# Performance work log

Measured on AMD Instinct MI355X. Metric: run time of the kernel, lower is better.

Reference implementation:

```python
import jax, jax.numpy as jnp
import numpy as np

N = 80
MAX_ITERS = 60   # fixed unroll; per-pair convergence handled by masking
TOL = 1e-3       # matches torch |ev - ev_new| < 0.001


def setup_inputs() -> dict:
    key = jax.random.key(0)
    k1, k2, k3, k4, k5, k6 = jax.random.split(key, 6)
    return {
        "x": jax.random.normal(k1, (N, 1), dtype=jnp.float32),
        "r_zeros": jax.random.uniform(k2, (N, N, N, N), dtype=jnp.float32),
        "r_const": jax.random.uniform(k3, (N, N, N, N), dtype=jnp.float32),
        "t_paths": jax.random.uniform(k4, (N, N), dtype=jnp.float32),
        "weights_t": jax.random.uniform(k5, (N, N), dtype=jnp.float32),
        "weights_r": jax.random.uniform(k6, (N, N, N, N), dtype=jnp.float32),
    }


def _batched_power_iteration(A):
    # A: [P, n, n]. Power iteration per pair, freezing converged pairs.
    P, n, _ = A.shape
    v0 = jnp.full((P, n), 1.0 / np.sqrt(n), dtype=A.dtype)

    def ev_fn(v):
        Av = jnp.einsum('pij,pj->pi', A, v)
        return jnp.einsum('pi,pi->p', v, Av)

    ev0 = ev_fn(v0)
    done0 = jnp.zeros((P,), dtype=bool)

    def body(carry, _):
        v, ev, done = carry
        Av = jnp.einsum('pij,pj->pi', A, v)
        v_new = Av / jnp.linalg.norm(Av, axis=1, keepdims=True)
        ev_new = ev_fn(v_new)
        conv = jnp.abs(ev - ev_new) < TOL
        # torch returns v_new at the converging step, then breaks
        v = jnp.where(done[:, None], v, v_new)
        ev = jnp.where(done, ev, ev_new)
        done = done | conv
        return (v, ev, done), None

    (v, ev, done), _ = jax.lax.scan(body, (v0, ev0, done0), None, length=MAX_ITERS)
    return ev, v


def reference(x, r_zeros, r_const, t_paths, weights_t, weights_r):
    n = x.shape[0]
    weights_t_fixed = weights_t * t_paths                      # [n, n]
    weights_r_comb = weights_r * r_zeros + r_const             # [n, n, n, n]

    A = weights_r_comb.reshape(n * n, n, n)                    # one matrix per (s,t)
    T_val = weights_t_fixed.reshape(n * n)                     # scalar per (s,t)
    src = jnp.repeat(jnp.arange(n), n)                         # s index per pair

    _, v = _batched_power_iteration(A)                         # [P, n]
    # compute_eigenvector_values: v / v[src] * T_val
    v_src = v[jnp.arange(n * n), src]                          # [P]
    deltas = v * (T_val / v_src)[:, None]                      # [P, n]
    rbc_arr = jnp.sum(deltas, axis=0)                          # [n]
    return rbc_arr
```

## Files before the change

### kernel.cpp

```cpp
#include <hip/hip_runtime.h>

#define NN 80
#define NPAIR (NN * NN)
#define MAXIT 60
#define TOLV 1e-3f

__device__ __forceinline__ float block_reduce_sum(float part, float* red) {
    const int lane = threadIdx.x & 63;
    const int wid  = threadIdx.x >> 6;
#pragma unroll
    for (int off = 32; off > 0; off >>= 1)
        part += __shfl_down(part, off, 64);
    if (lane == 0) red[wid] = part;
    __syncthreads();
    float r = red[0] + red[1] + red[2] + red[3];
    __syncthreads();
    return r;
}

template <bool ATOMIC>
__global__ __launch_bounds__(256) void pair_kernel(
    const float* __restrict__ r_zeros,
    const float* __restrict__ r_const,
    const float* __restrict__ t_paths,
    const float* __restrict__ weights_t,
    const float* __restrict__ weights_r,
    float* __restrict__ outbuf)
{
    __shared__ float A[NN][NN + 1];
    __shared__ float v[NN];
    __shared__ float Av[NN];
    __shared__ float red[4];

    const int p   = blockIdx.x;
    const int tid = threadIdx.x;
    const long base = (long)p * (NN * NN);

    const float4* wr4 = (const float4*)(weights_r + base);
    const float4* rz4 = (const float4*)(r_zeros + base);
    const float4* rc4 = (const float4*)(r_const + base);
    for (int c = tid; c < (NN * NN) / 4; c += 256) {
        float4 a = wr4[c];
        float4 b = rz4[c];
        float4 d = rc4[c];
        const int f = c * 4;
        const int row = f / NN, col = f % NN;
        A[row][col + 0] = fmaf(a.x, b.x, d.x);
        A[row][col + 1] = fmaf(a.y, b.y, d.y);
        A[row][col + 2] = fmaf(a.z, b.z, d.z);
        A[row][col + 3] = fmaf(a.w, b.w, d.w);
    }
    if (tid < NN) v[tid] = 0.11180339887498949f;
    __syncthreads();

    if (tid < NN) {
        float s = 0.f;
#pragma unroll
        for (int j = 0; j < NN; ++j) s = fmaf(A[tid][j], v[j], s);
        Av[tid] = s;
    }
    __syncthreads();
    float part = (tid < NN) ? v[tid] * Av[tid] : 0.f;
    float ev = block_reduce_sum(part, red);

    for (int it = 0; it < MAXIT; ++it) {
        part = (tid < NN) ? Av[tid] * Av[tid] : 0.f;
        const float inv = 1.f / sqrtf(block_reduce_sum(part, red));
        if (tid < NN) v[tid] = Av[tid] * inv;
        __syncthreads();
        if (tid < NN) {
            float s = 0.f;
#pragma unroll
            for (int j = 0; j < NN; ++j) s = fmaf(A[tid][j], v[j], s);
            Av[tid] = s;
        }
        __syncthreads();
        part = (tid < NN) ? v[tid] * Av[tid] : 0.f;
        const float ev_new = block_reduce_sum(part, red);
        if (fabsf(ev - ev_new) < TOLV) break;
        ev = ev_new;
    }

    const int s_idx = p / NN;
    const float T = weights_t[p] * t_paths[p];
    const float scale = T / v[s_idx];
    if (tid < NN) {
        const float dv = v[tid] * scale;
        if (ATOMIC) atomicAdd(&outbuf[tid], dv);
        else        outbuf[(long)p * NN + tid] = dv;
    }
}

__global__ __launch_bounds__(256) void reduce_kernel(
    const float* __restrict__ deltas, float* __restrict__ out)
{
    __shared__ float red[4];
    const int j = blockIdx.x;
    float part = 0.f;
    for (int p = threadIdx.x; p < NPAIR; p += 256)
        part += deltas[(long)p * NN + j];
    const int lane = threadIdx.x & 63;
    const int wid  = threadIdx.x >> 6;
#pragma unroll
    for (int off = 32; off > 0; off >>= 1)
        part += __shfl_down(part, off, 64);
    if (lane == 0) red[wid] = part;
    __syncthreads();
    if (threadIdx.x == 0) out[j] = red[0] + red[1] + red[2] + red[3];
}

extern "C" void kernel_launch(void* const* d_in, const int* in_sizes, int n_in,
                              void* d_out, int out_size, void* d_ws, size_t ws_size,
                              hipStream_t stream) {
    const float* r_zeros   = (const float*)d_in[1];
    const float* r_const   = (const float*)d_in[2];
    const float* t_paths   = (const float*)d_in[3];
    const float* weights_t = (const float*)d_in[4];
    const float* weights_r = (const float*)d_in[5];
    float* out = (float*)d_out;

    const size_t need = (size_t)NPAIR * NN * sizeof(float);
    if (ws_size >= need) {
        float* deltas = (float*)d_ws;
        pair_kernel<false><<<NPAIR, 256, 0, stream>>>(
            r_zeros, r_const, t_paths, weights_t, weights_r, deltas);
        reduce_kernel<<<NN, 256, 0, stream>>>(deltas, out);
    } else {
        hipMemsetAsync(d_out, 0, NN * sizeof(float), stream);
        pair_kernel<true><<<NPAIR, 256, 0, stream>>>(
            r_zeros, r_const, t_paths, weights_t, weights_r, out);
    }
}
```

Before: 443.5 us.

## Persistent double-buffered pair kernel overlapping next-matrix loads with power iteration

Replaces one-block-per-pair launch with a persistent grid of 768 blocks that loop over pairs, double-buffering the next pair's combined matrix in shared memory and interleaving chunks of its global load into the power-iteration steps. The matvec uses float4 reads with a rotated start index to avoid bank conflicts, and the two reductions per iteration are merged into one pass that also yields the norm for the next step. Results are accumulated with atomics instead of a workspace plus reduce kernel. The goal is to hide the HBM load latency behind the latency-bound iteration, at the cost of double shared memory and reduced occupancy.

```diff
diff --git a/kernel.cpp b/kernel.cpp
--- a/kernel.cpp
+++ b/kernel.cpp
@@ -1,112 +1,143 @@
 #include <hip/hip_runtime.h>
 
 #define NN 80
-#define NPAIR (NN * NN)
+#define NP4 1600
+#define NPAIR 6400
 #define MAXIT 60
 #define TOLV 1e-3f
+#define GRID 768
+#define NCHUNK 7
 
-__device__ __forceinline__ float block_reduce_sum(float part, float* red) {
-    const int lane = threadIdx.x & 63;
-    const int wid  = threadIdx.x >> 6;
+__device__ __forceinline__ float matvec_row(const float4* __restrict__ Ar4,
+                                            const float4* __restrict__ v4,
+                                            int q0) {
+    float s0 = 0.f, s1 = 0.f, s2 = 0.f, s3 = 0.f;
+    int q = q0;
 #pragma unroll
-    for (int off = 32; off > 0; off >>= 1)
-        part += __shfl_down(part, off, 64);
-    if (lane == 0) red[wid] = part;
-    __syncthreads();
-    float r = red[0] + red[1] + red[2] + red[3];
-    __syncthreads();
-    return r;
+    for (int c = 0; c < 20; ++c) {
+        const float4 a = Ar4[q];
+        const float4 w = v4[q];
+        s0 = fmaf(a.x, w.x, s0);
+        s1 = fmaf(a.y, w.y, s1);
+        s2 = fmaf(a.z, w.z, s2);
+        s3 = fmaf(a.w, w.w, s3);
+        q = (q == 19) ? 0 : q + 1;
+    }
+    return (s0 + s1) + (s2 + s3);
 }
 
-template <bool ATOMIC>
-__global__ __launch_bounds__(256) void pair_kernel(
+__global__ __launch_bounds__(256, 3) void pair_kernel(
     const float* __restrict__ r_zeros,
     const float* __restrict__ r_const,
     const float* __restrict__ t_paths,
     const float* __restrict__ weights_t,
     const float* __restrict__ weights_r,
-    float* __restrict__ outbuf)
+    float* __restrict__ out)
 {
-    __shared__ float A[NN][NN + 1];
+    __shared__ float A[2][NN * NN];
     __shared__ float v[NN];
-    __shared__ float Av[NN];
-    __shared__ float red[4];
+    __shared__ float red1[4], red2[4];
 
-    const int p   = blockIdx.x;
-    const int tid = threadIdx.x;
-    const long base = (long)p * (NN * NN);
+    const int tid  = threadIdx.x;
+    const int lane = tid & 63;
+    const int wid  = tid >> 6;
+    const int q0   = (tid < NN) ? (tid % 20) : 0;
 
-    const float4* wr4 = (const float4*)(weights_r + base);
-    const float4* rz4 = (const float4*)(r_zeros + base);
-    const float4* rc4 = (const float4*)(r_const + base);
-    for (int c = tid; c < (NN * NN) / 4; c += 256) {
-        float4 a = wr4[c];
-        float4 b = rz4[c];
-        float4 d = rc4[c];
-        const int f = c * 4;
-        const int row = f / NN, col = f % NN;
-        A[row][col + 0] = fmaf(a.x, b.x, d.x);
-        A[row][col + 1] = fmaf(a.y, b.y, d.y);
-        A[row][col + 2] = fmaf(a.z, b.z, d.z);
-        A[row][col + 3] = fmaf(a.w, b.w, d.w);
-    }
-    if (tid < NN) v[tid] = 0.11180339887498949f;
-    __syncthreads();
-
-    if (tid < NN) {
-        float s = 0.f;
-#pragma unroll
-        for (int j = 0; j < NN; ++j) s = fmaf(A[tid][j], v[j], s);
-        Av[tid] = s;
-    }
-    __syncthreads();
-    float part = (tid < NN) ? v[tid] * Av[tid] : 0.f;
-    float ev = block_reduce_sum(part, red);
-
-    for (int it = 0; it < MAXIT; ++it) {
-        part = (tid < NN) ? Av[tid] * Av[tid] : 0.f;
-        const float inv = 1.f / sqrtf(block_reduce_sum(part, red));
-        if (tid < NN) v[tid] = Av[tid] * inv;
-        __syncthreads();
-        if (tid < NN) {
-            float s = 0.f;
-#pragma unroll
-            for (int j = 0; j < NN; ++j) s = fmaf(A[tid][j], v[j], s);
-            Av[tid] = s;
+    {
+        const float4* wr4 = (const float4*)weights_r + (long)blockIdx.x * NP4;
+        const float4* rz4 = (const float4*)r_zeros  + (long)blockIdx.x * NP4;
+        const float4* rc4 = (const float4*)r_const  + (long)blockIdx.x * NP4;
+        for (int i4 = tid; i4 < NP4; i4 += 256) {
+            float4 a = wr4[i4], b = rz4[i4], d = rc4[i4];
+            float4 o;
+            o.x = fmaf(a.x, b.x, d.x);
+            o.y = fmaf(a.y, b.y, d.y);
+            o.z = fmaf(a.z, b.z, d.z);
+            o.w = fmaf(a.w, b.w, d.w);
+            *(float4*)&A[0][i4 * 4] = o;
         }
-        __syncthreads();
-        part = (tid < NN) ? v[tid] * Av[tid] : 0.f;
-        const float ev_new = block_reduce_sum(part, red);
-        if (fabsf(ev - ev_new) < TOLV) break;
-        ev = ev_new;
     }
 
-    const int s_idx = p / NN;
-    const float T = weights_t[p] * t_paths[p];
-    const float scale = T / v[s_idx];
-    if (tid < NN) {
-        const float dv = v[tid] * scale;
-        if (ATOMIC) atomicAdd(&outbuf[tid], dv);
-        else        outbuf[(long)p * NN + tid] = dv;
+    int cur = 0;
+    for (int p = blockIdx.x; p < NPAIR; p += GRID) {
+        const int  np = p + GRID;
+        const bool hn = np < NPAIR;
+        const float4* nwr = (const float4*)weights_r + (long)np * NP4;
+        const float4* nrz = (const float4*)r_zeros  + (long)np * NP4;
+        const float4* nrc = (const float4*)r_const  + (long)np * NP4;
+        float* nd = A[cur ^ 1];
+        int k = 0;
+        auto pf = [&]() {
+            if (hn && k < NCHUNK) {
+                const int i4 = k * 256 + tid;
+                if (i4 < NP4) {
+                    float4 a = nwr[i4], b = nrz[i4], d = nrc[i4];
+                    float4 o;
+                    o.x = fmaf(a.x, b.x, d.x);
+                    o.y = fmaf(a.y, b.y, d.y);
+                    o.z = fmaf(a.z, b.z, d.z);
+                    o.w = fmaf(a.w, b.w, d.w);
+                    *(float4*)&nd[i4 * 4] = o;
+                }
+                ++k;
+            }
+        };
+
+        const float4* Ar4 = (const float4*)&A[cur][tid * NN];
+        const float4* v4  = (const float4*)v;
+
+        if (tid < NN) v[tid] = 0.11180339887498949f;
+        __syncthreads();
+
+        float Avp = (tid < NN) ? matvec_row(Ar4, v4, q0) : 0.f;
+        float q1  = (tid < NN) ? v[tid] * Avp : 0.f;
+        float q2  = Avp * Avp;
+        pf();
+#pragma unroll
+        for (int off = 32; off; off >>= 1) {
+            q1 += __shfl_down(q1, off, 64);
+            q2 += __shfl_down(q2, off, 64);
+        }
+        if (lane == 0) { red1[wid] = q1; red2[wid] = q2; }
+        __syncthreads();
+        float ev   = (red1[0] + red1[1]) + (red1[2] + red1[3]);
+        float nrm2 = (red2[0] + red2[1]) + (red2[2] + red2[3]);
+        __syncthreads();
+
+        for (int it = 0; it < MAXIT; ++it) {
+            const float inv = 1.0f / sqrtf(nrm2);
+            if (tid < NN) v[tid] = Avp * inv;
+            pf();
+            __syncthreads();
+            Avp = (tid < NN) ? matvec_row(Ar4, v4, q0) : 0.f;
+            q1  = (tid < NN) ? v[tid] * Avp : 0.f;
+            q2  = Avp * Avp;
+            pf();
+#pragma unroll
+            for (int off = 32; off; off >>= 1) {
+                q1 += __shfl_down(q1, off, 64);
+                q2 += __shfl_down(q2, off, 64);
+            }
+            if (lane == 0) { red1[wid] = q1; red2[wid] = q2; }
+            __syncthreads();
+            const float ev_new   = (red1[0] + red1[1]) + (red1[2] + red1[3]);
+            const float nrm2_new = (red2[0] + red2[1]) + (red2[2] + red2[3]);
+            __syncthreads();
+            pf();
+            if (fabsf(ev - ev_new) < TOLV) break;
+            ev   = ev_new;
+            nrm2 = nrm2_new;
+        }
+
+        while (hn && k < NCHUNK) pf();
+        __syncthreads();
+
+        const float T     = weights_t[p] * t_paths[p];
+        const float scale = T / v[p / NN];
+        if (tid < NN) atomicAdd(&out[tid], v[tid] * scale);
+        __syncthreads();
+        cur ^= 1;
     }
-}
-
-__global__ __launch_bounds__(256) void reduce_kernel(
-    const float* __restrict__ deltas, float* __restrict__ out)
-{
-    __shared__ float red[4];
-    const int j = blockIdx.x;
-    float part = 0.f;
-    for (int p = threadIdx.x; p < NPAIR; p += 256)
-        part += deltas[(long)p * NN + j];
-    const int lane = threadIdx.x & 63;
-    const int wid  = threadIdx.x >> 6;
-#pragma unroll
-    for (int off = 32; off > 0; off >>= 1)
-        part += __shfl_down(part, off, 64);
-    if (lane == 0) red[wid] = part;
-    __syncthreads();
-    if (threadIdx.x == 0) out[j] = red[0] + red[1] + red[2] + red[3];
 }
 
 extern "C" void kernel_launch(void* const* d_in, const int* in_sizes, int n_in,
@@ -119,15 +150,7 @@
     const float* weights_r = (const float*)d_in[5];
     float* out = (float*)d_out;
 
-    const size_t need = (size_t)NPAIR * NN * sizeof(float);
-    if (ws_size >= need) {
-        float* deltas = (float*)d_ws;
-        pair_kernel<false><<<NPAIR, 256, 0, stream>>>(
-            r_zeros, r_const, t_paths, weights_t, weights_r, deltas);
-        reduce_kernel<<<NN, 256, 0, stream>>>(deltas, out);
-    } else {
-        hipMemsetAsync(d_out, 0, NN * sizeof(float), stream);
-        pair_kernel<true><<<NPAIR, 256, 0, stream>>>(
-            r_zeros, r_const, t_paths, weights_t, weights_r, out);
-    }
+    hipMemsetAsync(out, 0, NN * sizeof(float), stream);
+    pair_kernel<<<GRID, 256, 0, stream>>>(
+        r_zeros, r_const, t_paths, weights_t, weights_r, out);
 }
```

Measured after the change: 497.2 us. +12.1%, slower.

## Use single-wavefront blocks with bf16 shared matrix and register-resident power iteration

Applied to the files above, without the earlier changes.

Each pair's matrix is now stored in shared memory as bf16 instead of fp32, and each block shrinks to one 64-lane wavefront. Each lane owns one row, plus a second row for lanes below 16. The norm and eigenvalue reductions are fused into one shuffle-xor butterfly, which removes the shared-memory reduction buffer and most barriers. Row dot products use 16-byte vector loads with staggered starting offsets to spread LDS bank access. Halving LDS per block and cutting synchronisation is meant to raise occupancy and shorten each iteration, but bf16 storage of A lowers matrix precision and can change convergence behaviour.

```diff
diff --git a/kernel.cpp b/kernel.cpp
--- a/kernel.cpp
+++ b/kernel.cpp
@@ -1,25 +1,39 @@
 #include <hip/hip_runtime.h>
 
 #define NN 80
-#define NPAIR (NN * NN)
+#define NP4 1600
+#define NPAIR 6400
 #define MAXIT 60
 #define TOLV 1e-3f
 
-__device__ __forceinline__ float block_reduce_sum(float part, float* red) {
-    const int lane = threadIdx.x & 63;
-    const int wid  = threadIdx.x >> 6;
+__device__ __forceinline__ ushort f2bf(float x) {
+    unsigned u = __float_as_uint(x);
+    return (ushort)((u + 0x7FFFu + ((u >> 16) & 1u)) >> 16);
+}
+__device__ __forceinline__ float bflo(unsigned q) { return __uint_as_float(q << 16); }
+__device__ __forceinline__ float bfhi(unsigned q) { return __uint_as_float(q & 0xFFFF0000u); }
+
+__device__ __forceinline__ float rowdot(const ushort* __restrict__ Ab,
+                                        const float* __restrict__ vf, int r) {
+    const uint4* Ar = (const uint4*)(Ab + r * NN);
+    int k = r % 10;
+    float s0 = 0.f, s1 = 0.f, s2 = 0.f, s3 = 0.f;
 #pragma unroll
-    for (int off = 32; off > 0; off >>= 1)
-        part += __shfl_down(part, off, 64);
-    if (lane == 0) red[wid] = part;
-    __syncthreads();
-    float r = red[0] + red[1] + red[2] + red[3];
-    __syncthreads();
-    return r;
+    for (int c = 0; c < 10; ++c) {
+        const uint4 q = Ar[k];
+        const float4* vk = (const float4*)(vf + k * 8);
+        const float4 va = vk[0], vb = vk[1];
+        s0 = fmaf(bflo(q.x), va.x, s0);  s1 = fmaf(bfhi(q.x), va.y, s1);
+        s2 = fmaf(bflo(q.y), va.z, s2);  s3 = fmaf(bfhi(q.y), va.w, s3);
+        s0 = fmaf(bflo(q.z), vb.x, s0);  s1 = fmaf(bfhi(q.z), vb.y, s1);
+        s2 = fmaf(bflo(q.w), vb.z, s2);  s3 = fmaf(bfhi(q.w), vb.w, s3);
+        ++k; if (k == 10) k = 0;
+    }
+    return (s0 + s1) + (s2 + s3);
 }
 
-template <bool ATOMIC>
-__global__ __launch_bounds__(256) void pair_kernel(
+template <bool USE_WS>
+__global__ __launch_bounds__(64) void pair_kernel(
     const float* __restrict__ r_zeros,
     const float* __restrict__ r_const,
     const float* __restrict__ t_paths,
@@ -27,67 +41,74 @@
     const float* __restrict__ weights_r,
     float* __restrict__ outbuf)
 {
-    __shared__ float A[NN][NN + 1];
-    __shared__ float v[NN];
-    __shared__ float Av[NN];
-    __shared__ float red[4];
+    __shared__ __align__(16) ushort Ab[NN * NN];
+    __shared__ __align__(16) float  vf[NN];
 
-    const int p   = blockIdx.x;
-    const int tid = threadIdx.x;
-    const long base = (long)p * (NN * NN);
+    const int lane = threadIdx.x;
+    const int p    = blockIdx.x;
+    const long base4 = (long)p * NP4;
+    const float4* wr4 = (const float4*)weights_r + base4;
+    const float4* rz4 = (const float4*)r_zeros  + base4;
+    const float4* rc4 = (const float4*)r_const  + base4;
 
-    const float4* wr4 = (const float4*)(weights_r + base);
-    const float4* rz4 = (const float4*)(r_zeros + base);
-    const float4* rc4 = (const float4*)(r_const + base);
-    for (int c = tid; c < (NN * NN) / 4; c += 256) {
-        float4 a = wr4[c];
-        float4 b = rz4[c];
-        float4 d = rc4[c];
-        const int f = c * 4;
-        const int row = f / NN, col = f % NN;
-        A[row][col + 0] = fmaf(a.x, b.x, d.x);
-        A[row][col + 1] = fmaf(a.y, b.y, d.y);
-        A[row][col + 2] = fmaf(a.z, b.z, d.z);
-        A[row][col + 3] = fmaf(a.w, b.w, d.w);
+#pragma unroll 5
+    for (int kk = 0; kk < 25; ++kk) {
+        const int c = lane + kk * 64;
+        const float4 a = wr4[c], b = rz4[c], d = rc4[c];
+        ushort4 u;
+        u.x = f2bf(fmaf(a.x, b.x, d.x));
+        u.y = f2bf(fmaf(a.y, b.y, d.y));
+        u.z = f2bf(fmaf(a.z, b.z, d.z));
+        u.w = f2bf(fmaf(a.w, b.w, d.w));
+        *(ushort4*)&Ab[c * 4] = u;
     }
-    if (tid < NN) v[tid] = 0.11180339887498949f;
+    const float c0 = 0.11180339887498949f;
+    vf[lane] = c0;
+    if (lane < 16) vf[64 + lane] = c0;
     __syncthreads();
 
-    if (tid < NN) {
-        float s = 0.f;
+    float v1 = c0, v2 = (lane < 16) ? c0 : 0.f;
+    float a1 = rowdot(Ab, vf, lane);
+    float a2 = (lane < 16) ? rowdot(Ab, vf, 64 + lane) : 0.f;
+    float e = v1 * a1 + v2 * a2;
+    float n = a1 * a1 + a2 * a2;
 #pragma unroll
-        for (int j = 0; j < NN; ++j) s = fmaf(A[tid][j], v[j], s);
-        Av[tid] = s;
+    for (int off = 32; off; off >>= 1) {
+        e += __shfl_xor(e, off, 64);
+        n += __shfl_xor(n, off, 64);
     }
-    __syncthreads();
-    float part = (tid < NN) ? v[tid] * Av[tid] : 0.f;
-    float ev = block_reduce_sum(part, red);
+    float ev = e, nrm2 = n;
 
     for (int it = 0; it < MAXIT; ++it) {
-        part = (tid < NN) ? Av[tid] * Av[tid] : 0.f;
-        const float inv = 1.f / sqrtf(block_reduce_sum(part, red));
-        if (tid < NN) v[tid] = Av[tid] * inv;
+        const float inv = 1.f / sqrtf(nrm2);
+        v1 = a1 * inv; v2 = a2 * inv;
+        vf[lane] = v1;
+        if (lane < 16) vf[64 + lane] = v2;
         __syncthreads();
-        if (tid < NN) {
-            float s = 0.f;
+        a1 = rowdot(Ab, vf, lane);
+        a2 = (lane < 16) ? rowdot(Ab, vf, 64 + lane) : 0.f;
+        e = v1 * a1 + v2 * a2;
+        n = a1 * a1 + a2 * a2;
 #pragma unroll
-            for (int j = 0; j < NN; ++j) s = fmaf(A[tid][j], v[j], s);
-            Av[tid] = s;
+        for (int off = 32; off; off >>= 1) {
+            e += __shfl_xor(e, off, 64);
+            n += __shfl_xor(n, off, 64);
         }
-        __syncthreads();
-        part = (tid < NN) ? v[tid] * Av[tid] : 0.f;
-        const float ev_new = block_reduce_sum(part, red);
-        if (fabsf(ev - ev_new) < TOLV) break;
-        ev = ev_new;
+        if (fabsf(ev - e) < TOLV) break;
+        ev = e; nrm2 = n;
     }
 
     const int s_idx = p / NN;
-    const float T = weights_t[p] * t_paths[p];
-    const float scale = T / v[s_idx];
-    if (tid < NN) {
-        const float dv = v[tid] * scale;
-        if (ATOMIC) atomicAdd(&outbuf[tid], dv);
-        else        outbuf[(long)p * NN + tid] = dv;
+    const float vsrc = (s_idx < 64) ? __shfl(v1, s_idx, 64)
+                                    : __shfl(v2, s_idx - 64, 64);
+    const float scale = (weights_t[p] * t_paths[p]) / vsrc;
+    if (USE_WS) {
+        float* od = outbuf + (long)p * NN;
+        od[lane] = v1 * scale;
+        if (lane < 16) od[64 + lane] = v2 * scale;
+    } else {
+        atomicAdd(&outbuf[lane], v1 * scale);
+        if (lane < 16) atomicAdd(&outbuf[64 + lane], v2 * scale);
     }
 }
 
@@ -102,7 +123,7 @@
     const int lane = threadIdx.x & 63;
     const int wid  = threadIdx.x >> 6;
 #pragma unroll
-    for (int off = 32; off > 0; off >>= 1)
+    for (int off = 32; off; off >>= 1)
         part += __shfl_down(part, off, 64);
     if (lane == 0) red[wid] = part;
     __syncthreads();
@@ -122,12 +143,12 @@
     const size_t need = (size_t)NPAIR * NN * sizeof(float);
     if (ws_size >= need) {
         float* deltas = (float*)d_ws;
-        pair_kernel<false><<<NPAIR, 256, 0, stream>>>(
+        pair_kernel<true><<<NPAIR, 64, 0, stream>>>(
             r_zeros, r_const, t_paths, weights_t, weights_r, deltas);
         reduce_kernel<<<NN, 256, 0, stream>>>(deltas, out);
     } else {
-        hipMemsetAsync(d_out, 0, NN * sizeof(float), stream);
-        pair_kernel<true><<<NPAIR, 256, 0, stream>>>(
+        hipMemsetAsync(out, 0, NN * sizeof(float), stream);
+        pair_kernel<false><<<NPAIR, 64, 0, stream>>>(
             r_zeros, r_const, t_paths, weights_t, weights_r, out);
     }
 }
```

New measurement: 444.5 us. No clear change (+0.2%).
